# Optimization experiments

Hardware: AMD Instinct MI355X
Metric: run time of the kernel (lower is better)

The kernel has to match this reference:

```python
import jax, jax.numpy as jnp
import numpy as np

MAX_DISP = 1  # pad_size == max_displacement == 1


def setup_inputs() -> dict:
    key = jax.random.key(0)
    k1, k2 = jax.random.split(key)
    shape = (1, 64, 64, 128, 128)  # [B, C, D, H, W]
    in1 = jax.random.normal(k1, shape, dtype=jnp.float32)
    in2 = jax.random.normal(k2, shape, dtype=jnp.float32)
    return {"in1": in1, "in2": in2}


def reference(in1, in2):
    # zero-pad in2 by 1 on each side of D, H, W (ConstantPad3d(pad_size, 0))
    p = MAX_DISP
    in2_pad = jnp.pad(in2, ((0, 0), (0, 0), (p, p), (p, p), (p, p)))
    B, C, D, H, W = in1.shape
    n = 2 * p + 1
    outs = []
    # torch meshgrid(ij) over (z, y, x): dz varies slowest, dx fastest
    for dz in range(n):
        for dy in range(n):
            for dx in range(n):
                shifted = jax.lax.dynamic_slice(
                    in2_pad, (0, 0, dz, dy, dx), (B, C, D, H, W))
                # channel-mean of elementwise product -> [B, 1, D, H, W]
                outs.append(jnp.mean(in1 * shifted, axis=1, keepdims=True))
    return jnp.concatenate(outs, axis=1)  # [B, 27, D, H, W]
```

## Files before the change

kernel.cpp:

```cpp
#include <hip/hip_runtime.h>

constexpr int C  = 64;
constexpr int D  = 64;
constexpr int H  = 128;
constexpr int W  = 128;
constexpr int ZS = H * W;
constexpr int YS = W;
constexpr int CS = D * H * W;

__global__ __launch_bounds__(256)
void corr3d_kernel(const float* __restrict__ in1,
                   const float* __restrict__ in2,
                   float* __restrict__ out) {
    const int tx = threadIdx.x;
    const int ty = threadIdx.y;
    const int x0 = tx * 4;
    const int y  = blockIdx.x * 8 + ty;
    const int z  = blockIdx.y;

    float acc[27][4];
#pragma unroll
    for (int j = 0; j < 27; ++j) {
#pragma unroll
        for (int i = 0; i < 4; ++i) acc[j][i] = 0.0f;
    }

    const float* p1 = in1 + z * ZS + y * YS + x0;
    const bool xlo = (x0 > 0);
    const bool xhi = (x0 < W - 4);

    for (int c = 0; c < C; ++c) {
        const float4 a = *(const float4*)(p1 + c * CS);

#pragma unroll
        for (int dz = 0; dz < 3; ++dz) {
            const int zz = z + dz - 1;
            const bool zok = ((unsigned)zz < (unsigned)D);
#pragma unroll
            for (int dy = 0; dy < 3; ++dy) {
                const int yy = y + dy - 1;
                const bool ok = zok && ((unsigned)yy < (unsigned)H);

                float v0, v1, v2, v3, v4, v5;
                if (ok) {
                    const float* p = in2 + c * CS + zz * ZS + yy * YS + x0;
                    const float4 m = *(const float4*)p;
                    v1 = m.x; v2 = m.y; v3 = m.z; v4 = m.w;
                    v0 = xlo ? p[-1] : 0.0f;
                    v5 = xhi ? p[4]  : 0.0f;
                } else {
                    v0 = v1 = v2 = v3 = v4 = v5 = 0.0f;
                }

                const int jb = (dz * 3 + dy) * 3;
                acc[jb + 0][0] += a.x * v0;
                acc[jb + 0][1] += a.y * v1;
                acc[jb + 0][2] += a.z * v2;
                acc[jb + 0][3] += a.w * v3;

                acc[jb + 1][0] += a.x * v1;
                acc[jb + 1][1] += a.y * v2;
                acc[jb + 1][2] += a.z * v3;
                acc[jb + 1][3] += a.w * v4;

                acc[jb + 2][0] += a.x * v2;
                acc[jb + 2][1] += a.y * v3;
                acc[jb + 2][2] += a.z * v4;
                acc[jb + 2][3] += a.w * v5;
            }
        }
    }

    const float s = 1.0f / (float)C;
    float* po = out + z * ZS + y * YS + x0;
#pragma unroll
    for (int j = 0; j < 27; ++j) {
        float4 o;
        o.x = acc[j][0] * s;
        o.y = acc[j][1] * s;
        o.z = acc[j][2] * s;
        o.w = acc[j][3] * s;
        *(float4*)(po + (size_t)j * CS) = o;
    }
}

extern "C" void kernel_launch(void* const* d_in, const int* in_sizes, int n_in,
                              void* d_out, int out_size, void* d_ws, size_t ws_size,
                              hipStream_t stream) {
    const float* in1 = (const float*)d_in[0];
    const float* in2 = (const float*)d_in[1];
    float* out = (float*)d_out;

    dim3 block(32, 8);
    dim3 grid(H / 8, D);
    corr3d_kernel<<<grid, block, 0, stream>>>(in1, in2, out);
}
```

Measured before the change: 752.2 us.

## Make in2 loads branchless with clamped row offsets and masks, batch loads per channel

Precomputes clamped row offsets and 0/1 masks for the nine (dz,dy) neighbour rows so every in2 load is unconditional, and issues all nine float4 loads plus edge scalars before the FMAs. in1 loads and output stores become nontemporal, and launch bounds request two blocks per SIMD. The goal is to remove divergent branches and raise memory-level parallelism. The cost is extra multiplies for masking, redundant loads at boundaries, and higher register pressure that may cause spills under the new occupancy bound.

New measurement: 818.1 us. +8.8%, slower.

```diff
diff --git a/kernel.cpp b/kernel.cpp
--- a/kernel.cpp
+++ b/kernel.cpp
@@ -8,7 +8,9 @@
 constexpr int YS = W;
 constexpr int CS = D * H * W;
 
-__global__ __launch_bounds__(256)
+typedef float f4 __attribute__((ext_vector_type(4)));
+
+__global__ __launch_bounds__(256, 2)
 void corr3d_kernel(const float* __restrict__ in1,
                    const float* __restrict__ in2,
                    float* __restrict__ out) {
@@ -25,49 +27,72 @@
         for (int i = 0; i < 4; ++i) acc[j][i] = 0.0f;
     }
 
-    const float* p1 = in1 + z * ZS + y * YS + x0;
+    int   rowoff[9];
+    float rowmask[9];
+#pragma unroll
+    for (int dz = 0; dz < 3; ++dz) {
+        const int zz  = z + dz - 1;
+        const int zzc = min(max(zz, 0), D - 1);
+        const bool zok = ((unsigned)zz < (unsigned)D);
+#pragma unroll
+        for (int dy = 0; dy < 3; ++dy) {
+            const int yy  = y + dy - 1;
+            const int yyc = min(max(yy, 0), H - 1);
+            const bool ok = zok && ((unsigned)yy < (unsigned)H);
+            const int r = dz * 3 + dy;
+            rowoff[r]  = zzc * ZS + yyc * YS + x0;
+            rowmask[r] = ok ? 1.0f : 0.0f;
+        }
+    }
+
     const bool xlo = (x0 > 0);
     const bool xhi = (x0 < W - 4);
+    const int   offm = xlo ? -1 : 0;
+    const int   offp = xhi ?  4 : 3;
+    const float mlo  = xlo ? 1.0f : 0.0f;
+    const float mhi  = xhi ? 1.0f : 0.0f;
+
+    const float* p1 = in1 + z * ZS + y * YS + x0;
 
     for (int c = 0; c < C; ++c) {
-        const float4 a = *(const float4*)(p1 + c * CS);
+        const float* b2 = in2 + c * CS;
+
+        const f4 a = __builtin_nontemporal_load((const f4*)(p1 + c * CS));
+
+        f4    m[9];
+        float vl[9], vr[9];
+#pragma unroll
+        for (int r = 0; r < 9; ++r) {
+            const float* p = b2 + rowoff[r];
+            m[r]  = *(const f4*)p;
+            vl[r] = p[offm];
+            vr[r] = p[offp];
+        }
 
 #pragma unroll
-        for (int dz = 0; dz < 3; ++dz) {
-            const int zz = z + dz - 1;
-            const bool zok = ((unsigned)zz < (unsigned)D);
-#pragma unroll
-            for (int dy = 0; dy < 3; ++dy) {
-                const int yy = y + dy - 1;
-                const bool ok = zok && ((unsigned)yy < (unsigned)H);
+        for (int r = 0; r < 9; ++r) {
+            const float msk = rowmask[r];
+            const float ax = a.x * msk, ay = a.y * msk,
+                        az = a.z * msk, aw = a.w * msk;
+            const float v0 = vl[r] * mlo;
+            const float v1 = m[r].x, v2 = m[r].y, v3 = m[r].z, v4 = m[r].w;
+            const float v5 = vr[r] * mhi;
+            const int jb = r * 3;
 
-                float v0, v1, v2, v3, v4, v5;
-                if (ok) {
-                    const float* p = in2 + c * CS + zz * ZS + yy * YS + x0;
-                    const float4 m = *(const float4*)p;
-                    v1 = m.x; v2 = m.y; v3 = m.z; v4 = m.w;
-                    v0 = xlo ? p[-1] : 0.0f;
-                    v5 = xhi ? p[4]  : 0.0f;
-                } else {
-                    v0 = v1 = v2 = v3 = v4 = v5 = 0.0f;
-                }
+            acc[jb + 0][0] += ax * v0;
+            acc[jb + 0][1] += ay * v1;
+            acc[jb + 0][2] += az * v2;
+            acc[jb + 0][3] += aw * v3;
 
-                const int jb = (dz * 3 + dy) * 3;
-                acc[jb + 0][0] += a.x * v0;
-                acc[jb + 0][1] += a.y * v1;
-                acc[jb + 0][2] += a.z * v2;
-                acc[jb + 0][3] += a.w * v3;
+            acc[jb + 1][0] += ax * v1;
+            acc[jb + 1][1] += ay * v2;
+            acc[jb + 1][2] += az * v3;
+            acc[jb + 1][3] += aw * v4;
 
-                acc[jb + 1][0] += a.x * v1;
-                acc[jb + 1][1] += a.y * v2;
-                acc[jb + 1][2] += a.z * v3;
-                acc[jb + 1][3] += a.w * v4;
-
-                acc[jb + 2][0] += a.x * v2;
-                acc[jb + 2][1] += a.y * v3;
-                acc[jb + 2][2] += a.z * v4;
-                acc[jb + 2][3] += a.w * v5;
-            }
+            acc[jb + 2][0] += ax * v2;
+            acc[jb + 2][1] += ay * v3;
+            acc[jb + 2][2] += az * v4;
+            acc[jb + 2][3] += aw * v5;
         }
     }
 
@@ -75,12 +100,12 @@
     float* po = out + z * ZS + y * YS + x0;
 #pragma unroll
     for (int j = 0; j < 27; ++j) {
-        float4 o;
+        f4 o;
         o.x = acc[j][0] * s;
         o.y = acc[j][1] * s;
         o.z = acc[j][2] * s;
         o.w = acc[j][3] * s;
-        *(float4*)(po + (size_t)j * CS) = o;
+        __builtin_nontemporal_store(o, (f4*)(po + (size_t)j * CS));
     }
 }
 
```
